# Optimization experiments

Measured on AMD Instinct MI355X. Metric: run time of the kernel, lower is better.

The kernel has to match this reference:

```python
import jax, jax.numpy as jnp
import numpy as np

B, S, D, H = 4, 2048, 1024, 16
HD = D // H  # 64


def setup_inputs() -> dict:
    key = jax.random.key(0)
    ks = jax.random.split(key, 16)
    inv = 1.0 / np.sqrt(D)
    inv_hd = 1.0 / np.sqrt(D)
    inp = {
        "query": jax.random.normal(ks[0], (B, S, D), jnp.float32),
        "key": jax.random.normal(ks[1], (B, S, D), jnp.float32),
        "value": jax.random.normal(ks[2], (B, S, D), jnp.float32),
        # causal mask: True entries are masked out (masked_fill semantics)
        "mask": jnp.triu(jnp.ones((S, S), jnp.bool_), k=1),
        # weights stored [in, out] (math identical to torch x @ W.T)
        "Wq": jax.random.normal(ks[3], (D, D), jnp.float32) * inv,
        "Wk": jax.random.normal(ks[4], (D, D), jnp.float32) * inv,
        "Wv": jax.random.normal(ks[5], (D, D), jnp.float32) * inv,
        "wq_h": jax.random.normal(ks[6], (D, HD), jnp.float32) * inv_hd,
        "bq_h": jax.random.normal(ks[7], (HD,), jnp.float32) * inv_hd,
        "wk_h": jax.random.normal(ks[8], (D, HD), jnp.float32) * inv_hd,
        "bk_h": jax.random.normal(ks[9], (HD,), jnp.float32) * inv_hd,
        "wv_h": jax.random.normal(ks[10], (D, HD), jnp.float32) * inv_hd,
        "bv_h": jax.random.normal(ks[11], (HD,), jnp.float32) * inv_hd,
        "Wo": jax.random.normal(ks[12], (D, D), jnp.float32) * inv,
    }
    return inp


def reference(query, key, value, mask, Wq, Wk, Wv, wq_h, bq_h, wk_h, bk_h, wv_h, bv_h, Wo):
    # full-width projections
    q = jnp.einsum('bsd,de->bse', query, Wq)
    k = jnp.einsum('bsd,de->bse', key, Wk)
    v = jnp.einsum('bsd,de->bse', value, Wv)
    # per-head projections: the torch loop reuses the SAME weights every
    # iteration, so all H head outputs are identical -> compute once.
    qh = jnp.einsum('bsd,dh->bsh', q, wq_h) + bq_h  # [B,S,HD]
    kh = jnp.einsum('bsd,dh->bsh', k, wk_h) + bk_h
    vh = jnp.einsum('bsd,dh->bsh', v, wv_h) + bv_h
    scores = jnp.einsum('bsh,bth->bst', qh, kh) / jnp.sqrt(jnp.float32(HD))
    scores = jnp.where(mask, jnp.float32(-1e9), scores)
    attn = jax.nn.softmax(scores, axis=-1)
    out_h = jnp.einsum('bst,bth->bsh', attn, vh)  # [B,S,HD]
    out = jnp.tile(out_h, (1, 1, H))  # cat of H identical heads -> [B,S,D]
    # final linear; dropout is identity at inference
    return jnp.einsum('bsd,de->bse', out, Wo)
```

## Files before the change

kernel.cpp:

```cpp
#include <hip/hip_runtime.h>
#include <math.h>

#define S_LEN 2048
#define BATCH 4
#define DMODEL 1024
#define HDIM 64
#define NROWS (BATCH * S_LEN)

typedef __attribute__((ext_vector_type(8))) short bf16x8;
typedef __attribute__((ext_vector_type(4))) float f32x4;

__device__ inline ushort f2bf(float f) {
    union { float f; uint u; } v{f};
    uint r = v.u + 0x7fffu + ((v.u >> 16) & 1u);
    return (ushort)(r >> 16);
}

__device__ inline bf16x8 cvt8(float4 a, float4 b) {
    bf16x8 r;
    r[0] = (short)f2bf(a.x); r[1] = (short)f2bf(a.y);
    r[2] = (short)f2bf(a.z); r[3] = (short)f2bf(a.w);
    r[4] = (short)f2bf(b.x); r[5] = (short)f2bf(b.y);
    r[6] = (short)f2bf(b.z); r[7] = (short)f2bf(b.w);
    return r;
}

__global__ __launch_bounds__(256) void transpose_wh(
    const float* __restrict__ B0, const float* __restrict__ B1, const float* __restrict__ B2,
    ushort* __restrict__ T0, ushort* __restrict__ T1, ushort* __restrict__ T2)
{
    const int z = blockIdx.y;
    const float* B = (z == 0) ? B0 : (z == 1) ? B1 : B2;
    ushort* T      = (z == 0) ? T0 : (z == 1) ? T1 : T2;
    const int kr0 = blockIdx.x * 64;
    __shared__ ushort Ts[64][72];
    const int t = threadIdx.x;

    #pragma unroll
    for (int q = 0; q < 4; ++q) {
        int u   = t * 4 + q;
        int row = u >> 4;
        int c4  = (u & 15) << 2;
        float4 v = *reinterpret_cast<const float4*>(
            B + (size_t)(kr0 + row) * 64 + c4);
        Ts[row][c4 + 0] = f2bf(v.x); Ts[row][c4 + 1] = f2bf(v.y);
        Ts[row][c4 + 2] = f2bf(v.z); Ts[row][c4 + 3] = f2bf(v.w);
    }
    __syncthreads();
    #pragma unroll
    for (int q = 0; q < 2; ++q) {
        int u  = t * 2 + q;
        int h  = u >> 3;
        int k8 = (u & 7) << 3;
        uint4 o;
        uint* ow = reinterpret_cast<uint*>(&o);
        #pragma unroll
        for (int i = 0; i < 4; ++i)
            ow[i] = (uint)Ts[k8 + 2 * i][h] | ((uint)Ts[k8 + 2 * i + 1][h] << 16);
        *reinterpret_cast<uint4*>(T + (size_t)h * 1024 + kr0 + k8) = o;
    }
}

__global__ __launch_bounds__(256, 6) void prep_direct(
    const float* __restrict__ A0, const float* __restrict__ A1, const float* __restrict__ A2,
    const ushort* __restrict__ W0, const ushort* __restrict__ W1, const ushort* __restrict__ W2,
    ushort* __restrict__ T0, ushort* __restrict__ T1, ushort* __restrict__ T2)
{
    const int z = blockIdx.y;
    const float* A  = (z == 0) ? A0 : (z == 1) ? A1 : A2;
    const ushort* W = (z == 0) ? W0 : (z == 1) ? W1 : W2;
    ushort* T       = (z == 0) ? T0 : (z == 1) ? T1 : T2;

    __shared__ float Pr[4][16][64];

    const int t    = threadIdx.x;
    const int w    = t >> 6;
    const int lane = t & 63;
    const int lg   = lane >> 4;
    const int lc   = lane & 15;
    const int r0   = blockIdx.x * 16;

    const float*  Ap = A + (size_t)(r0 + lc) * 1024 + (w << 8) + (lg << 3);
    const ushort* Bp = W + (size_t)lc * 1024 + (w << 8) + (lg << 3);

    f32x4 acc[4] = {};
    float4 a0[2], a1[2];
    uint4  bl[2][4];

    #pragma unroll
    for (int d = 0; d < 2; ++d) {
        a0[d] = *reinterpret_cast<const float4*>(Ap + d * 32);
        a1[d] = *reinterpret_cast<const float4*>(Ap + d * 32 + 4);
        #pragma unroll
        for (int n = 0; n < 4; ++n)
            bl[d][n] = *reinterpret_cast<const uint4*>(Bp + n * 16384 + d * 32);
    }

    #pragma unroll
    for (int ks = 0; ks < 8; ++ks) {
        const int d = ks & 1;
        bf16x8 af = cvt8(a0[d], a1[d]);
        bf16x8 bfr[4];
        #pragma unroll
        for (int n = 0; n < 4; ++n)
            bfr[n] = __builtin_bit_cast(bf16x8, bl[d][n]);
        if (ks < 6) {
            a0[d] = *reinterpret_cast<const float4*>(Ap + (ks + 2) * 32);
            a1[d] = *reinterpret_cast<const float4*>(Ap + (ks + 2) * 32 + 4);
            #pragma unroll
            for (int n = 0; n < 4; ++n)
                bl[d][n] = *reinterpret_cast<const uint4*>(Bp + n * 16384 + (ks + 2) * 32);
        }
        #pragma unroll
        for (int n = 0; n < 4; ++n)
            acc[n] = __builtin_amdgcn_mfma_f32_16x16x32_bf16(af, bfr[n], acc[n], 0, 0, 0);
    }

    #pragma unroll
    for (int n = 0; n < 4; ++n)
        #pragma unroll
        for (int reg = 0; reg < 4; ++reg)
            Pr[w][4 * lg + reg][16 * n + lc] = acc[n][reg];
    __syncthreads();

    const int row = t >> 4;
    const int col = (t & 15) << 2;
    float s[4];
    #pragma unroll
    for (int i = 0; i < 4; ++i)
        s[i] = Pr[0][row][col + i] + Pr[1][row][col + i] +
               Pr[2][row][col + i] + Pr[3][row][col + i];
    #pragma unroll
    for (int i = 0; i < 4; ++i)
        T[(size_t)(col + i) * 1024 + r0 + row] = f2bf(s[i]);
}

__global__ __launch_bounds__(256, 6) void proj_direct(
    const float* __restrict__ A0, const float* __restrict__ A1, const float* __restrict__ A2,
    const ushort* __restrict__ W0, const ushort* __restrict__ W1, const ushort* __restrict__ W2,
    const float* __restrict__ b0, const float* __restrict__ b1, const float* __restrict__ b2,
    ushort* __restrict__ O0, ushort* __restrict__ O1, ushort* __restrict__ O2)
{
    const int z = blockIdx.y;
    const float* A    = (z == 0) ? A0 : (z == 1) ? A1 : A2;
    const ushort* W   = (z == 0) ? W0 : (z == 1) ? W1 : W2;
    const float* bias = (z == 0) ? b0 : (z == 1) ? b1 : b2;
    ushort* O         = (z == 0) ? O0 : (z == 1) ? O1 : O2;

    __shared__ float Pr[4][16][64];

    const int t    = threadIdx.x;
    const int w    = t >> 6;
    const int lane = t & 63;
    const int lg   = lane >> 4;
    const int lc   = lane & 15;
    const int r0   = blockIdx.x * 16;

    const float*  Ap = A + (size_t)(r0 + lc) * 1024 + (w << 8) + (lg << 3);
    const ushort* Bp = W + (size_t)lc * 1024 + (w << 8) + (lg << 3);

    f32x4 acc[4] = {};
    float4 a0[2], a1[2];
    uint4  bl[2][4];

    #pragma unroll
    for (int d = 0; d < 2; ++d) {
        a0[d] = *reinterpret_cast<const float4*>(Ap + d * 32);
        a1[d] = *reinterpret_cast<const float4*>(Ap + d * 32 + 4);
        #pragma unroll
        for (int n = 0; n < 4; ++n)
            bl[d][n] = *reinterpret_cast<const uint4*>(Bp + n * 16384 + d * 32);
    }

    #pragma unroll
    for (int ks = 0; ks < 8; ++ks) {
        const int d = ks & 1;
        bf16x8 af = cvt8(a0[d], a1[d]);
        bf16x8 bfr[4];
        #pragma unroll
        for (int n = 0; n < 4; ++n)
            bfr[n] = __builtin_bit_cast(bf16x8, bl[d][n]);
        if (ks < 6) {
            a0[d] = *reinterpret_cast<const float4*>(Ap + (ks + 2) * 32);
            a1[d] = *reinterpret_cast<const float4*>(Ap + (ks + 2) * 32 + 4);
            #pragma unroll
            for (int n = 0; n < 4; ++n)
                bl[d][n] = *reinterpret_cast<const uint4*>(Bp + n * 16384 + (ks + 2) * 32);
        }
        #pragma unroll
        for (int n = 0; n < 4; ++n)
            acc[n] = __builtin_amdgcn_mfma_f32_16x16x32_bf16(af, bfr[n], acc[n], 0, 0, 0);
    }

    #pragma unroll
    for (int n = 0; n < 4; ++n)
        #pragma unroll
        for (int reg = 0; reg < 4; ++reg)
            Pr[w][4 * lg + reg][16 * n + lc] = acc[n][reg];
    __syncthreads();

    const int row = t >> 4;
    const int col = (t & 15) << 2;
    float4 bb = *reinterpret_cast<const float4*>(bias + col);
    float s0 = Pr[0][row][col + 0] + Pr[1][row][col + 0] + Pr[2][row][col + 0] + Pr[3][row][col + 0] + bb.x;
    float s1 = Pr[0][row][col + 1] + Pr[1][row][col + 1] + Pr[2][row][col + 1] + Pr[3][row][col + 1] + bb.y;
    float s2 = Pr[0][row][col + 2] + Pr[1][row][col + 2] + Pr[2][row][col + 2] + Pr[3][row][col + 2] + bb.z;
    float s3 = Pr[0][row][col + 3] + Pr[1][row][col + 3] + Pr[2][row][col + 3] + Pr[3][row][col + 3] + bb.w;
    ushort4 o;
    o.x = f2bf(s0); o.y = f2bf(s1); o.z = f2bf(s2); o.w = f2bf(s3);
    *reinterpret_cast<ushort4*>(O + (size_t)(r0 + row) * 64 + col) = o;
}

__global__ __launch_bounds__(256) void fold_wo(const float* __restrict__ Wo,
                                               ushort* __restrict__ WoT)
{
    int idx = blockIdx.x * 256 + threadIdx.x;
    int j = idx >> 10;
    int e = idx & 1023;
    float s = 0.f;
    #pragma unroll
    for (int h = 0; h < 16; ++h)
        s += Wo[(size_t)((h << 6) + j) * 1024 + e];
    WoT[(size_t)e * 64 + j] = f2bf(s);
}

__global__ __launch_bounds__(256) void transpose_v(const ushort* __restrict__ vh,
                                                   ushort* __restrict__ vhT)
{
    const int b  = blockIdx.y;
    const int r0 = blockIdx.x * 64;
    __shared__ ushort T[64][72];
    const int t = threadIdx.x;

    #pragma unroll
    for (int q = 0; q < 2; ++q) {
        int u  = t * 2 + q;
        int s  = u >> 3;
        int d8 = (u & 7) << 3;
        uint4 v = *reinterpret_cast<const uint4*>(
            vh + ((size_t)b * S_LEN + r0 + s) * 64 + d8);
        *reinterpret_cast<uint4*>(&T[s][d8]) = v;
    }
    __syncthreads();
    #pragma unroll
    for (int q = 0; q < 2; ++q) {
        int u  = t * 2 + q;
        int d  = u >> 3;
        int s8 = (u & 7) << 3;
        uint4 o;
        uint* ow = reinterpret_cast<uint*>(&o);
        #pragma unroll
        for (int i = 0; i < 4; ++i)
            ow[i] = (uint)T[s8 + 2 * i][d] | ((uint)T[s8 + 2 * i + 1][d] << 16);
        *reinterpret_cast<uint4*>(
            vhT + (size_t)b * 64 * S_LEN + (size_t)d * S_LEN + r0 + s8) = o;
    }
}

__global__ __launch_bounds__(256) void flash_mfma(
    const ushort* __restrict__ qh, const ushort* __restrict__ kh,
    const ushort* __restrict__ vhT,
    float* __restrict__ Opart, float* __restrict__ mpart, float* __restrict__ lpart)
{
    const int b = blockIdx.y;
    const int u = blockIdx.x;
    int gi = 0;
    #pragma unroll
    for (int gg = 0; gg < 7; ++gg)
        if (u >= 2 * (gg + 1) * (gg + 2)) gi = gg + 1;
    const int rem = u - 2 * gi * (gi + 1);
    const int dq  = rem / (gi + 1);
    const int c   = rem - dq * (gi + 1);
    const int qt  = 4 * gi + dq;
    const int r0  = qt * 64;
    const int kvbase = c << 8;
    const int slot = b * 144 + u;

    __shared__ ushort Qs[64][72];
    __shared__ ushort Ks[64][72];
    __shared__ ushort Vt[64][72];
    __shared__ ushort Pw[4][16][72];

    const int t    = threadIdx.x;
    const int w    = t >> 6;
    const int lane = t & 63;
    const int lg   = lane >> 4;
    const int lc   = lane & 15;

    const ushort* qb  = qh  + (size_t)b * S_LEN * 64;
    const ushort* kb  = kh  + (size_t)b * S_LEN * 64;
    const ushort* vtb = vhT + (size_t)b * 64 * S_LEN;

    #pragma unroll
    for (int q = 0; q < 2; ++q) {
        int uu  = t * 2 + q;
        int row = uu >> 3;
        int c8  = (uu & 7) << 3;
        *reinterpret_cast<uint4*>(&Qs[row][c8]) =
            *reinterpret_cast<const uint4*>(qb + (size_t)(r0 + row) * 64 + c8);
    }
    __syncthreads();
    bf16x8 qf0 = *reinterpret_cast<const bf16x8*>(&Qs[16 * w + lc][lg * 8]);
    bf16x8 qf1 = *reinterpret_cast<const bf16x8*>(&Qs[16 * w + lc][32 + lg * 8]);

    f32x4 od[4] = {};
    float m = -INFINITY, lsum = 0.f;
    const int qrow = r0 + 16 * w + lc;

    const int ntt = min(4, ((r0 + 63 - kvbase) >> 6) + 1);
    for (int tt = 0; tt < ntt; ++tt) {
        const int t0 = kvbase + (tt << 6);
        __syncthreads();
        #pragma unroll
        for (int q = 0; q < 2; ++q) {
            int uu  = t * 2 + q;
            int row = uu >> 3;
            int c8  = (uu & 7) << 3;
            *reinterpret_cast<uint4*>(&Ks[row][c8]) =
                *reinterpret_cast<const uint4*>(kb + (size_t)(t0 + row) * 64 + c8);
            *reinterpret_cast<uint4*>(&Vt[row][c8]) =
                *reinterpret_cast<const uint4*>(vtb + (size_t)row * S_LEN + t0 + c8);
        }
        __syncthreads();

        if (t0 <= r0 + 16 * w + 15) {
            f32x4 s[4] = {};
            #pragma unroll
            for (int a = 0; a < 4; ++a) {
                bf16x8 kf0 = *reinterpret_cast<const bf16x8*>(&Ks[16 * a + lc][lg * 8]);
                bf16x8 kf1 = *reinterpret_cast<const bf16x8*>(&Ks[16 * a + lc][32 + lg * 8]);
                s[a] = __builtin_amdgcn_mfma_f32_16x16x32_bf16(kf0, qf0, s[a], 0, 0, 0);
                s[a] = __builtin_amdgcn_mfma_f32_16x16x32_bf16(kf1, qf1, s[a], 0, 0, 0);
            }
            float rm = -1e30f;
            #pragma unroll
            for (int a = 0; a < 4; ++a)
                #pragma unroll
                for (int reg = 0; reg < 4; ++reg) {
                    int kv = t0 + 16 * a + 4 * lg + reg;
                    float v = s[a][reg] * 0.125f;
                    if (kv > qrow) v = -1e30f;
                    s[a][reg] = v;
                    rm = fmaxf(rm, v);
                }
            rm = fmaxf(rm, __shfl_xor(rm, 16));
            rm = fmaxf(rm, __shfl_xor(rm, 32));
            float mn = fmaxf(m, rm);
            float sc = __expf(m - mn);
            float rs = 0.f;
            #pragma unroll
            for (int a = 0; a < 4; ++a)
                #pragma unroll
                for (int reg = 0; reg < 4; ++reg) {
                    float p = __expf(s[a][reg] - mn);
                    s[a][reg] = p;
                    rs += p;
                }
            rs += __shfl_xor(rs, 16);
            rs += __shfl_xor(rs, 32);
            lsum = lsum * sc + rs;
            m = mn;
            #pragma unroll
            for (int di = 0; di < 4; ++di) od[di] *= sc;

            #pragma unroll
            for (int a = 0; a < 4; ++a)
                #pragma unroll
                for (int rp = 0; rp < 2; ++rp) {
                    uint pk = (uint)f2bf(s[a][2 * rp]) |
                              ((uint)f2bf(s[a][2 * rp + 1]) << 16);
                    *reinterpret_cast<uint*>(&Pw[w][lc][16 * a + 4 * lg + 2 * rp]) = pk;
                }
            bf16x8 pf0 = *reinterpret_cast<const bf16x8*>(&Pw[w][lc][lg * 8]);
            bf16x8 pf1 = *reinterpret_cast<const bf16x8*>(&Pw[w][lc][32 + lg * 8]);
            #pragma unroll
            for (int di = 0; di < 4; ++di) {
                bf16x8 vf0 = *reinterpret_cast<const bf16x8*>(&Vt[16 * di + lc][lg * 8]);
                bf16x8 vf1 = *reinterpret_cast<const bf16x8*>(&Vt[16 * di + lc][32 + lg * 8]);
                od[di] = __builtin_amdgcn_mfma_f32_16x16x32_bf16(vf0, pf0, od[di], 0, 0, 0);
                od[di] = __builtin_amdgcn_mfma_f32_16x16x32_bf16(vf1, pf1, od[di], 0, 0, 0);
            }
        }
    }

    #pragma unroll
    for (int di = 0; di < 4; ++di)
        #pragma unroll
        for (int reg = 0; reg < 4; ++reg)
            Opart[(size_t)slot * 4096 + (16 * di + 4 * lg + reg) * 64 + 16 * w + lc] =
                od[di][reg];
    if (lg == 0) {
        mpart[slot * 64 + 16 * w + lc] = m;
        lpart[slot * 64 + 16 * w + lc] = lsum;
    }
}

__global__ __launch_bounds__(256) void flash_combine(
    const float* __restrict__ Opart, const float* __restrict__ mpart,
    const float* __restrict__ lpart, ushort* __restrict__ oh)
{
    const int qt = blockIdx.x, b = blockIdx.y;
    const int gi = qt >> 2;
    const int nc = gi + 1;
    const int ubase = 2 * gi * (gi + 1) + (qt & 3) * (gi + 1);
    __shared__ float T[64][65];

    const int t  = threadIdx.x;
    const int q  = t & 63;
    const int d0 = (t >> 6) << 4;

    float mc[8];
    float M = -INFINITY;
    #pragma unroll
    for (int cc = 0; cc < 8; ++cc) {
        mc[cc] = (cc < nc) ? mpart[(b * 144 + ubase + cc) * 64 + q] : -INFINITY;
        M = fmaxf(M, mc[cc]);
    }
    float L = 0.f;
    float acc[16] = {};
    for (int cc = 0; cc < nc; ++cc) {
        const int slot = b * 144 + ubase + cc;
        float wgt = __expf(mc[cc] - M);
        L += lpart[slot * 64 + q] * wgt;
        const float* op = Opart + (size_t)slot * 4096 + q;
        #pragma unroll
        for (int i = 0; i < 16; ++i)
            acc[i] += wgt * op[(d0 + i) * 64];
    }
    float inv = 1.f / L;
    #pragma unroll
    for (int i = 0; i < 16; ++i) T[q][d0 + i] = acc[i] * inv;
    __syncthreads();

    const int q2 = t >> 2;
    const int ds = (t & 3) << 4;
    uint wbuf[8];
    #pragma unroll
    for (int i = 0; i < 8; ++i)
        wbuf[i] = (uint)f2bf(T[q2][ds + 2 * i]) |
                  ((uint)f2bf(T[q2][ds + 2 * i + 1]) << 16);
    ushort* dst = oh + ((size_t)b * S_LEN + qt * 64 + q2) * 64 + ds;
    uint4 o1, o2;
    o1.x = wbuf[0]; o1.y = wbuf[1]; o1.z = wbuf[2]; o1.w = wbuf[3];
    o2.x = wbuf[4]; o2.y = wbuf[5]; o2.z = wbuf[6]; o2.w = wbuf[7];
    *reinterpret_cast<uint4*>(dst)     = o1;
    *reinterpret_cast<uint4*>(dst + 8) = o2;
}

__global__ __launch_bounds__(256) void epilogue_mfma(
    const ushort* __restrict__ oh, const ushort* __restrict__ WoT,
    float* __restrict__ out)
{
    const int r0 = blockIdx.x * 64;
    const int c0 = blockIdx.y * 128;
    __shared__ ushort As[64][72];
    __shared__ ushort Bs[128][72];

    const int t    = threadIdx.x;
    const int w    = t >> 6;
    const int lane = t & 63;
    const int lg   = lane >> 4;
    const int lc   = lane & 15;

    #pragma unroll
    for (int q = 0; q < 2; ++q) {
        int u   = t * 2 + q;
        int row = u >> 3;
        int c8  = (u & 7) << 3;
        *reinterpret_cast<uint4*>(&As[row][c8]) =
            *reinterpret_cast<const uint4*>(oh + (size_t)(r0 + row) * 64 + c8);
    }
    #pragma unroll
    for (int q = 0; q < 4; ++q) {
        int u   = t * 4 + q;
        int row = u >> 3;
        int c8  = (u & 7) << 3;
        *reinterpret_cast<uint4*>(&Bs[row][c8]) =
            *reinterpret_cast<const uint4*>(WoT + (size_t)(c0 + row) * 64 + c8);
    }
    __syncthreads();

    bf16x8 af0 = *reinterpret_cast<const bf16x8*>(&As[16 * w + lc][lg * 8]);
    bf16x8 af1 = *reinterpret_cast<const bf16x8*>(&As[16 * w + lc][32 + lg * 8]);
    f32x4 acc[8] = {};
    #pragma unroll
    for (int n = 0; n < 8; ++n) {
        bf16x8 bf0 = *reinterpret_cast<const bf16x8*>(&Bs[16 * n + lc][lg * 8]);
        bf16x8 bf1 = *reinterpret_cast<const bf16x8*>(&Bs[16 * n + lc][32 + lg * 8]);
        acc[n] = __builtin_amdgcn_mfma_f32_16x16x32_bf16(af0, bf0, acc[n], 0, 0, 0);
        acc[n] = __builtin_amdgcn_mfma_f32_16x16x32_bf16(af1, bf1, acc[n], 0, 0, 0);
    }
    #pragma unroll
    for (int n = 0; n < 8; ++n)
        #pragma unroll
        for (int reg = 0; reg < 4; ++reg)
            out[(size_t)(r0 + 16 * w + 4 * lg + reg) * 1024 + c0 + 16 * n + lc] =
                acc[n][reg];
}

extern "C" void kernel_launch(void* const* d_in, const int* in_sizes, int n_in,
                              void* d_out, int out_size, void* d_ws, size_t ws_size,
                              hipStream_t stream)
{
    const float* query = (const float*)d_in[0];
    const float* key   = (const float*)d_in[1];
    const float* value = (const float*)d_in[2];
    const float* Wq   = (const float*)d_in[4];
    const float* Wk   = (const float*)d_in[5];
    const float* Wv   = (const float*)d_in[6];
    const float* wq_h = (const float*)d_in[7];
    const float* bq_h = (const float*)d_in[8];
    const float* wk_h = (const float*)d_in[9];
    const float* bk_h = (const float*)d_in[10];
    const float* wv_h = (const float*)d_in[11];
    const float* bv_h = (const float*)d_in[12];
    const float* Wo   = (const float*)d_in[13];
    float* out = (float*)d_out;

    ushort* W16  = (ushort*)d_ws;
    ushort* WT0  = W16;
    ushort* WT1  = W16 + 65536;
    ushort* WT2  = W16 + 131072;
    ushort* WoT  = W16 + 196608;
    ushort* qh   = W16 + 262144;
    ushort* kh   = qh + 524288;
    ushort* vh   = kh + 524288;
    ushort* vhT  = vh + 524288;
    ushort* oh   = vhT + 524288;
    ushort* whT0 = oh + 524288;
    ushort* whT1 = whT0 + 65536;
    ushort* whT2 = whT1 + 65536;

    float* Opart = out;
    float* mpart = out + 2359296;
    float* lpart = out + 2396160;

    transpose_wh<<<dim3(16, 3), 256, 0, stream>>>(
        wq_h, wk_h, wv_h, whT0, whT1, whT2);
    fold_wo<<<256, 256, 0, stream>>>(Wo, WoT);

    prep_direct<<<dim3(64, 3), 256, 0, stream>>>(
        Wq, Wk, Wv, whT0, whT1, whT2, WT0, WT1, WT2);

    proj_direct<<<dim3(512, 3), 256, 0, stream>>>(
        query, key, value, WT0, WT1, WT2, bq_h, bk_h, bv_h, qh, kh, vh);

    transpose_v<<<dim3(S_LEN / 64, BATCH), 256, 0, stream>>>(vh, vhT);

    flash_mfma<<<dim3(144, BATCH), 256, 0, stream>>>(
        qh, kh, vhT, Opart, mpart, lpart);
    flash_combine<<<dim3(S_LEN / 64, BATCH), 256, 0, stream>>>(
        Opart, mpart, lpart, oh);

    epilogue_mfma<<<dim3(NROWS / 64, DMODEL / 128), 256, 0, stream>>>(oh, WoT, out);
}
```

Before: 84.20 us.

## Stage fp32 activations via global_load_lds into swizzled LDS for projection GEMMs

```diff
diff --git a/kernel.cpp b/kernel.cpp
--- a/kernel.cpp
+++ b/kernel.cpp
@@ -9,6 +9,9 @@
 
 typedef __attribute__((ext_vector_type(8))) short bf16x8;
 typedef __attribute__((ext_vector_type(4))) float f32x4;
+
+#define GLP(p) ((const __attribute__((address_space(1))) unsigned int*)(p))
+#define LDP(p) ((__attribute__((address_space(3))) unsigned int*)(p))
 
 __device__ inline ushort f2bf(float f) {
     union { float f; uint u; } v{f};
@@ -61,81 +64,56 @@
     }
 }
 
-__global__ __launch_bounds__(256, 6) void prep_direct(
-    const float* __restrict__ A0, const float* __restrict__ A1, const float* __restrict__ A2,
-    const ushort* __restrict__ W0, const ushort* __restrict__ W1, const ushort* __restrict__ W2,
-    ushort* __restrict__ T0, ushort* __restrict__ T1, ushort* __restrict__ T2)
-{
-    const int z = blockIdx.y;
-    const float* A  = (z == 0) ? A0 : (z == 1) ? A1 : A2;
-    const ushort* W = (z == 0) ? W0 : (z == 1) ? W1 : W2;
-    ushort* T       = (z == 0) ? T0 : (z == 1) ? T1 : T2;
-
-    __shared__ float Pr[4][16][64];
-
-    const int t    = threadIdx.x;
-    const int w    = t >> 6;
-    const int lane = t & 63;
-    const int lg   = lane >> 4;
-    const int lc   = lane & 15;
-    const int r0   = blockIdx.x * 16;
-
-    const float*  Ap = A + (size_t)(r0 + lc) * 1024 + (w << 8) + (lg << 3);
-    const ushort* Bp = W + (size_t)lc * 1024 + (w << 8) + (lg << 3);
-
-    f32x4 acc[4] = {};
-    float4 a0[2], a1[2];
-    uint4  bl[2][4];
-
-    #pragma unroll
-    for (int d = 0; d < 2; ++d) {
-        a0[d] = *reinterpret_cast<const float4*>(Ap + d * 32);
-        a1[d] = *reinterpret_cast<const float4*>(Ap + d * 32 + 4);
-        #pragma unroll
-        for (int n = 0; n < 4; ++n)
-            bl[d][n] = *reinterpret_cast<const uint4*>(Bp + n * 16384 + d * 32);
-    }
-
-    #pragma unroll
-    for (int ks = 0; ks < 8; ++ks) {
-        const int d = ks & 1;
-        bf16x8 af = cvt8(a0[d], a1[d]);
-        bf16x8 bfr[4];
-        #pragma unroll
-        for (int n = 0; n < 4; ++n)
-            bfr[n] = __builtin_bit_cast(bf16x8, bl[d][n]);
-        if (ks < 6) {
-            a0[d] = *reinterpret_cast<const float4*>(Ap + (ks + 2) * 32);
-            a1[d] = *reinterpret_cast<const float4*>(Ap + (ks + 2) * 32 + 4);
-            #pragma unroll
-            for (int n = 0; n < 4; ++n)
-                bl[d][n] = *reinterpret_cast<const uint4*>(Bp + n * 16384 + (ks + 2) * 32);
-        }
-        #pragma unroll
-        for (int n = 0; n < 4; ++n)
-            acc[n] = __builtin_amdgcn_mfma_f32_16x16x32_bf16(af, bfr[n], acc[n], 0, 0, 0);
-    }
-
-    #pragma unroll
-    for (int n = 0; n < 4; ++n)
-        #pragma unroll
-        for (int reg = 0; reg < 4; ++reg)
-            Pr[w][4 * lg + reg][16 * n + lc] = acc[n][reg];
-    __syncthreads();
-
-    const int row = t >> 4;
-    const int col = (t & 15) << 2;
-    float s[4];
-    #pragma unroll
-    for (int i = 0; i < 4; ++i)
-        s[i] = Pr[0][row][col + i] + Pr[1][row][col + i] +
-               Pr[2][row][col + i] + Pr[3][row][col + i];
-    #pragma unroll
-    for (int i = 0; i < 4; ++i)
-        T[(size_t)(col + i) * 1024 + r0 + row] = f2bf(s[i]);
-}
-
-__global__ __launch_bounds__(256, 6) void proj_direct(
+#define GEMM_CORE(A, W, r0)                                                     \
+    __shared__ __align__(16) float As[2048];                                    \
+    const int t    = threadIdx.x;                                               \
+    const int w    = t >> 6;                                                    \
+    const int lane = t & 63;                                                    \
+    const int lg   = lane >> 4;                                                 \
+    const int lc   = lane & 15;                                                 \
+    const int rowH  = (w & 1) << 4;                                             \
+    const int npair = (w >> 1) << 1;                                            \
+    const int idx0 = t * 4;                                                     \
+    const int row0 = idx0 >> 6, g0 = (idx0 >> 2) & 15;                          \
+    const int idx1 = idx0 + 1024;                                               \
+    const int row1 = idx1 >> 6, g1 = (idx1 >> 2) & 15;                          \
+    const float* s0 = A + (size_t)(r0 + row0) * 1024 + ((g0 ^ (row0 & 7)) << 2);\
+    const float* s1 = A + (size_t)(r0 + row1) * 1024 + ((g1 ^ (row1 & 7)) << 2);\
+    char* l0 = (char*)As + t * 16;                                              \
+    char* l1 = (char*)As + t * 16 + 4096;                                       \
+    const ushort* Wb0 = W + (size_t)(16 * npair + lc) * 1024 + lg * 8;          \
+    const ushort* Wb1 = Wb0 + 16 * 1024;                                        \
+    f32x4 acc[2] = {};                                                          \
+    const int row  = rowH + lc;                                                 \
+    const int base = row * 16;                                                  \
+    const int rx   = lc & 7;                                                    \
+    const float4* Af4 = reinterpret_cast<const float4*>(As);                    \
+    for (int k0 = 0; k0 < 1024; k0 += 64) {                                     \
+        __builtin_amdgcn_global_load_lds(GLP(s0 + k0), LDP(l0), 16, 0, 0);      \
+        __builtin_amdgcn_global_load_lds(GLP(s1 + k0), LDP(l1), 16, 0, 0);      \
+        uint4 b00 = *reinterpret_cast<const uint4*>(Wb0 + k0);                  \
+        uint4 b01 = *reinterpret_cast<const uint4*>(Wb0 + k0 + 32);             \
+        uint4 b10 = *reinterpret_cast<const uint4*>(Wb1 + k0);                  \
+        uint4 b11 = *reinterpret_cast<const uint4*>(Wb1 + k0 + 32);             \
+        __syncthreads();                                                        \
+        float4 fa00 = Af4[base + ((lg * 2    ) ^ rx)];                          \
+        float4 fa01 = Af4[base + ((lg * 2 + 1) ^ rx)];                          \
+        float4 fa10 = Af4[base + ((lg * 2 + 8) ^ rx)];                          \
+        float4 fa11 = Af4[base + ((lg * 2 + 9) ^ rx)];                          \
+        bf16x8 a0 = cvt8(fa00, fa01);                                           \
+        bf16x8 a1 = cvt8(fa10, fa11);                                           \
+        acc[0] = __builtin_amdgcn_mfma_f32_16x16x32_bf16(                       \
+            a0, __builtin_bit_cast(bf16x8, b00), acc[0], 0, 0, 0);              \
+        acc[0] = __builtin_amdgcn_mfma_f32_16x16x32_bf16(                       \
+            a1, __builtin_bit_cast(bf16x8, b01), acc[0], 0, 0, 0);              \
+        acc[1] = __builtin_amdgcn_mfma_f32_16x16x32_bf16(                       \
+            a0, __builtin_bit_cast(bf16x8, b10), acc[1], 0, 0, 0);              \
+        acc[1] = __builtin_amdgcn_mfma_f32_16x16x32_bf16(                       \
+            a1, __builtin_bit_cast(bf16x8, b11), acc[1], 0, 0, 0);              \
+        __syncthreads();                                                        \
+    }
+
+__global__ __launch_bounds__(256) void proj_gl(
     const float* __restrict__ A0, const float* __restrict__ A1, const float* __restrict__ A2,
     const ushort* __restrict__ W0, const ushort* __restrict__ W1, const ushort* __restrict__ W2,
     const float* __restrict__ b0, const float* __restrict__ b1, const float* __restrict__ b2,
@@ -146,69 +124,39 @@
     const ushort* W   = (z == 0) ? W0 : (z == 1) ? W1 : W2;
     const float* bias = (z == 0) ? b0 : (z == 1) ? b1 : b2;
     ushort* O         = (z == 0) ? O0 : (z == 1) ? O1 : O2;
-
-    __shared__ float Pr[4][16][64];
-
-    const int t    = threadIdx.x;
-    const int w    = t >> 6;
-    const int lane = t & 63;
-    const int lg   = lane >> 4;
-    const int lc   = lane & 15;
-    const int r0   = blockIdx.x * 16;
-
-    const float*  Ap = A + (size_t)(r0 + lc) * 1024 + (w << 8) + (lg << 3);
-    const ushort* Bp = W + (size_t)lc * 1024 + (w << 8) + (lg << 3);
-
-    f32x4 acc[4] = {};
-    float4 a0[2], a1[2];
-    uint4  bl[2][4];
-
-    #pragma unroll
-    for (int d = 0; d < 2; ++d) {
-        a0[d] = *reinterpret_cast<const float4*>(Ap + d * 32);
-        a1[d] = *reinterpret_cast<const float4*>(Ap + d * 32 + 4);
-        #pragma unroll
-        for (int n = 0; n < 4; ++n)
-            bl[d][n] = *reinterpret_cast<const uint4*>(Bp + n * 16384 + d * 32);
-    }
-
-    #pragma unroll
-    for (int ks = 0; ks < 8; ++ks) {
-        const int d = ks & 1;
-        bf16x8 af = cvt8(a0[d], a1[d]);
-        bf16x8 bfr[4];
-        #pragma unroll
-        for (int n = 0; n < 4; ++n)
-            bfr[n] = __builtin_bit_cast(bf16x8, bl[d][n]);
-        if (ks < 6) {
-            a0[d] = *reinterpret_cast<const float4*>(Ap + (ks + 2) * 32);
-            a1[d] = *reinterpret_cast<const float4*>(Ap + (ks + 2) * 32 + 4);
-            #pragma unroll
-            for (int n = 0; n < 4; ++n)
-                bl[d][n] = *reinterpret_cast<const uint4*>(Bp + n * 16384 + (ks + 2) * 32);
-        }
-        #pragma unroll
-        for (int n = 0; n < 4; ++n)
-            acc[n] = __builtin_amdgcn_mfma_f32_16x16x32_bf16(af, bfr[n], acc[n], 0, 0, 0);
-    }
-
-    #pragma unroll
-    for (int n = 0; n < 4; ++n)
+    const int r0 = blockIdx.x * 32;
+
+    GEMM_CORE(A, W, r0)
+
+    float bv0 = bias[16 * npair + lc];
+    float bv1 = bias[16 * npair + 16 + lc];
+    #pragma unroll
+    for (int reg = 0; reg < 4; ++reg) {
+        int orow = r0 + rowH + 4 * lg + reg;
+        O[(size_t)orow * 64 + 16 * npair + lc]      = f2bf(acc[0][reg] + bv0);
+        O[(size_t)orow * 64 + 16 * npair + 16 + lc] = f2bf(acc[1][reg] + bv1);
+    }
+}
+
+__global__ __launch_bounds__(256) void prep_gl(
+    const float* __restrict__ A0, const float* __restrict__ A1, const float* __restrict__ A2,
+    const ushort* __restrict__ W0, const ushort* __restrict__ W1, const ushort* __restrict__ W2,
+    ushort* __restrict__ T0, ushort* __restrict__ T1, ushort* __restrict__ T2)
+{
+    const int z = blockIdx.y;
+    const float* A  = (z == 0) ? A0 : (z == 1) ? A1 : A2;
+    const ushort* W = (z == 0) ? W0 : (z == 1) ? W1 : W2;
+    ushort* T       = (z == 0) ? T0 : (z == 1) ? T1 : T2;
+    const int r0 = blockIdx.x * 32;
+
+    GEMM_CORE(A, W, r0)
+
+    #pragma unroll
+    for (int n = 0; n < 2; ++n)
         #pragma unroll
         for (int reg = 0; reg < 4; ++reg)
-            Pr[w][4 * lg + reg][16 * n + lc] = acc[n][reg];
-    __syncthreads();
-
-    const int row = t >> 4;
-    const int col = (t & 15) << 2;
-    float4 bb = *reinterpret_cast<const float4*>(bias + col);
-    float s0 = Pr[0][row][col + 0] + Pr[1][row][col + 0] + Pr[2][row][col + 0] + Pr[3][row][col + 0] + bb.x;
-    float s1 = Pr[0][row][col + 1] + Pr[1][row][col + 1] + Pr[2][row][col + 1] + Pr[3][row][col + 1] + bb.y;
-    float s2 = Pr[0][row][col + 2] + Pr[1][row][col + 2] + Pr[2][row][col + 2] + Pr[3][row][col + 2] + bb.z;
-    float s3 = Pr[0][row][col + 3] + Pr[1][row][col + 3] + Pr[2][row][col + 3] + Pr[3][row][col + 3] + bb.w;
-    ushort4 o;
-    o.x = f2bf(s0); o.y = f2bf(s1); o.z = f2bf(s2); o.w = f2bf(s3);
-    *reinterpret_cast<ushort4*>(O + (size_t)(r0 + row) * 64 + col) = o;
+            T[(size_t)(16 * (npair + n) + lc) * 1024 + (r0 + rowH + 4 * lg + reg)] =
+                f2bf(acc[n][reg]);
 }
 
 __global__ __launch_bounds__(256) void fold_wo(const float* __restrict__ Wo,
@@ -539,10 +487,10 @@
         wq_h, wk_h, wv_h, whT0, whT1, whT2);
     fold_wo<<<256, 256, 0, stream>>>(Wo, WoT);
 
-    prep_direct<<<dim3(64, 3), 256, 0, stream>>>(
+    prep_gl<<<dim3(32, 3), 256, 0, stream>>>(
         Wq, Wk, Wv, whT0, whT1, whT2, WT0, WT1, WT2);
 
-    proj_direct<<<dim3(512, 3), 256, 0, stream>>>(
+    proj_gl<<<dim3(256, 3), 256, 0, stream>>>(
         query, key, value, WT0, WT1, WT2, bq_h, bk_h, bv_h, qh, kh, vh);
 
     transpose_v<<<dim3(S_LEN / 64, BATCH), 256, 0, stream>>>(vh, vhT);
```

Result: no change. 85.21 us (+1.2%).
